# Kernel tuning notes

Hardware: AMD Instinct MI355X
Metric: run time of the kernel (lower is better)

## Reference

```python
import jax, jax.numpy as jnp
import numpy as np

B, L, V, OOV, E, H = 16, 256, 50000, 100, 128, 128
PAD_IDX, PLACEHOLDER_IDX = 0, 1


def lstm(x, W_ih, W_hh, b):
    # x: (B, T, I) -> hidden states (B, T, H); PyTorch gate order i,f,g,o
    nh = W_hh.shape[1]
    xg = jnp.einsum('bti,gi->btg', x, W_ih) + b  # precompute input gates

    def step(carry, xt):
        h, c = carry
        g = xt + h @ W_hh.T
        i, f, gg, o = jnp.split(g, 4, axis=-1)
        c = jax.nn.sigmoid(f) * c + jax.nn.sigmoid(i) * jnp.tanh(gg)
        h = jax.nn.sigmoid(o) * jnp.tanh(c)
        return (h, c), h

    bsz = x.shape[0]
    init = (jnp.zeros((bsz, nh), x.dtype), jnp.zeros((bsz, nh), x.dtype))
    _, hs = jax.lax.scan(step, init, jnp.swapaxes(xg, 0, 1))
    return jnp.swapaxes(hs, 0, 1)


def setup_inputs() -> dict:
    key = jax.random.key(0)
    ks = jax.random.split(key, 20)
    s = 0.05
    return {
        'src_tokens': jax.random.randint(ks[0], (B, L), 2, V),
        'src_lens': jnp.full((B,), L, dtype=jnp.int64 if jax.config.jax_enable_x64 else jnp.int32),
        'prev_output_tokens': jax.random.randint(ks[1], (B, 1), 2, V),
        'prev_output_lens': jnp.ones((B,), jnp.int32),
        'src_tokens_with_oov': jax.random.randint(ks[2], (B, L), 2, V + OOV),
        'oov_counts': jax.random.randint(ks[3], (B,), 0, OOV + 1),
        'decoder_state': jax.random.normal(ks[4], (B, H), jnp.float32),
        'embedding': jax.random.normal(ks[5], (V, E), jnp.float32) * 0.02,
        'enc_W_ih': jax.random.normal(ks[6], (4 * H, E), jnp.float32) * s,
        'enc_W_hh': jax.random.normal(ks[7], (4 * H, H), jnp.float32) * s,
        'enc_b': jnp.zeros((4 * H,), jnp.float32),
        'dec_W_ih': jax.random.normal(ks[8], (4 * H, E + H), jnp.float32) * s,
        'dec_W_hh': jax.random.normal(ks[9], (4 * H, H), jnp.float32) * s,
        'dec_b': jnp.zeros((4 * H,), jnp.float32),
        'attn_W': jax.random.normal(ks[10], (H, H), jnp.float32) * s,
        'out_W': jax.random.normal(ks[11], (H, 2 * H), jnp.float32) * s,
        'out_b': jnp.zeros((H,), jnp.float32),
        'copy_W': jax.random.normal(ks[12], (H, H), jnp.float32) * s,
        'gen_W': jax.random.normal(ks[13], (V + OOV, H), jnp.float32) * 0.02,
    }


def reference(src_tokens, src_lens, prev_output_tokens, prev_output_lens,
              src_tokens_with_oov, oov_counts, decoder_state,
              embedding, enc_W_ih, enc_W_hh, enc_b,
              dec_W_ih, dec_W_hh, dec_b,
              attn_W, out_W, out_b, copy_W, gen_W):
    neg_inf = -jnp.inf
    # ---- encoder ----
    enc_out = lstm(embedding[src_tokens], enc_W_ih, enc_W_hh, enc_b)  # B,L,H
    pad_mask = src_tokens == PAD_IDX                                   # B,L

    # ---- copy-state attention (selective read) ----
    mask = (prev_output_tokens == src_tokens).astype(enc_out.dtype)[..., None]  # B,L,1
    agg_w = jnp.tanh(jnp.einsum('blh,gh->blg', mask * enc_out, copy_W))
    cw = jax.nn.softmax(jnp.einsum('blg,bg->bl', agg_w, decoder_state), axis=1)
    copy_state = jnp.einsum('bl,blh->bh', cw, enc_out)

    # ---- decoder LSTM single step ----
    src_embed = embedding[prev_output_tokens[:, 0]]                    # B,E
    dec_in = jnp.concatenate([src_embed, copy_state], -1)[:, None, :]
    rnn_out = lstm(dec_in, dec_W_ih, dec_W_hh, dec_b)[:, 0]           # B,H

    # ---- attention ----
    scores = jnp.einsum('bh,blh->bl', rnn_out @ attn_W.T, enc_out)
    scores = jnp.where(pad_mask, neg_inf, scores)
    aw = jax.nn.softmax(scores, axis=1)
    ctx = jnp.einsum('bl,blh->bh', aw, enc_out)
    attn_out = jnp.tanh(jnp.concatenate([rnn_out, ctx], -1) @ out_W.T + out_b)

    # ---- generate + copy logits ----
    gen_logits = attn_out @ gen_W.T                                    # B,V+OOV
    b_idx = jnp.broadcast_to(jnp.arange(B)[:, None], (B, L))
    # scatter-reduce: equivalent to dense src_map (B, V+OOV, L) @ enc_out
    agg = jnp.zeros((B, V + OOV, H), enc_out.dtype).at[b_idx, src_tokens_with_oov].add(enc_out)
    copy_wts = jnp.tanh(jnp.einsum('bvh,gh->bvg', agg, copy_W))
    copy_score = jnp.einsum('bvg,bg->bv', copy_wts, attn_out)
    pos = jnp.arange(V + OOV)[None]
    copy_score = jnp.where(pos >= V + oov_counts[:, None], neg_inf, copy_score)

    total = gen_logits + copy_score
    total = jnp.where(pos == PLACEHOLDER_IDX, neg_inf, total)
    total_prob = jax.nn.softmax(total, axis=1)
    return total_prob, enc_out, attn_out
```

## Files before the change

### kernel.cpp

```cpp
#include <hip/hip_runtime.h>
#include <math.h>

#define B_   16
#define L_   256
#define V_   50000
#define NV_  50100
#define E_   128
#define H_   128
#define G4_  512
#define CHUNK_ 1566

typedef float f32x4 __attribute__((ext_vector_type(4)));
typedef float f32x2 __attribute__((ext_vector_type(2)));

__device__ __forceinline__ float sigm(float x){ return 1.0f/(1.0f+__expf(-x)); }
__device__ __forceinline__ float tanh_fast(float x){
  x = fminf(15.0f, fmaxf(-15.0f, x));
  float t = __expf(2.0f*x);
  return (t-1.0f)/(t+1.0f);
}

__global__ __launch_bounds__(512) void enc_xg_kernel(
    const int* __restrict__ tok, const float* __restrict__ emb,
    const float* __restrict__ Wih, const float* __restrict__ bias,
    float* __restrict__ xg)
{
  __shared__ __align__(16) float sx[16*128];
  int r0 = blockIdx.x*16;
  int t = threadIdx.x;
  for (int i=t; i<16*128; i+=512){
    int r=i>>7, e=i&127;
    sx[i] = emb[(size_t)tok[r0+r]*E_ + e];
  }
  __syncthreads();
  int g = t;
  float acc[16];
  #pragma unroll
  for (int r=0;r<16;r++) acc[r]=0.f;
  const f32x4* wr = (const f32x4*)(Wih + (size_t)g*E_);
  #pragma unroll 2
  for (int i=0;i<32;i++){
    f32x4 w = wr[i];
    #pragma unroll
    for (int r=0;r<16;r++){
      f32x4 x = ((const f32x4*)(sx + r*128))[i];
      acc[r] += w.x*x.x + w.y*x.y + w.z*x.z + w.w*x.w;
    }
  }
  float bg = bias[g];
  #pragma unroll
  for (int r=0;r<16;r++) xg[(size_t)(r0+r)*G4_ + g] = acc[r] + bg;
}

__global__ __launch_bounds__(512, 2) void enc_lstm_kernel(
    const float* __restrict__ xg, const float* __restrict__ Whh,
    float* __restrict__ enc_out)
{
  int b = blockIdx.x;
  int g = threadIdx.x;
  f32x2 w2[64];
  {
    const f32x4* wr4 = (const f32x4*)(Whh + (size_t)g*H_);
    #pragma unroll
    for (int k=0;k<32;k++){
      f32x4 wv = wr4[k];
      w2[2*k]   = wv.xy;
      w2[2*k+1] = wv.zw;
    }
  }
  #pragma unroll
  for (int k=0;k<64;k++) asm volatile("" : "+v"(w2[k]));

  __shared__ __align__(16) float sh_h[128];
  __shared__ float sh_g[512];
  if (g<128) sh_h[g]=0.f;
  float c = 0.f;
  const float* xgb = xg + (size_t)b*L_*G4_;
  float* eob = enc_out + (size_t)b*L_*H_;
  __syncthreads();

  const f32x4* sh4 = (const f32x4*)sh_h;
  bool is_gg = (g>=256 && g<384);
  float xcur = xgb[g];
  for (int t=0;t<L_;t++){
    float xnext = (t<L_-1) ? xgb[(t+1)*G4_ + g] : 0.f;
    f32x2 a0 = {xcur, 0.f}, a1 = {0.f,0.f}, a2 = {0.f,0.f}, a3 = {0.f,0.f};
    #pragma unroll
    for (int k=0;k<32;k+=4){
      f32x4 h0=sh4[k], h1=sh4[k+1], h2v=sh4[k+2], h3=sh4[k+3];
      a0 += w2[2*k+0]*h0.xy;  a1 += w2[2*k+1]*h0.zw;
      a2 += w2[2*k+2]*h1.xy;  a3 += w2[2*k+3]*h1.zw;
      a0 += w2[2*k+4]*h2v.xy; a1 += w2[2*k+5]*h2v.zw;
      a2 += w2[2*k+6]*h3.xy;  a3 += w2[2*k+7]*h3.zw;
    }
    f32x2 as = (a0+a1)+(a2+a3);
    float acc = as.x + as.y;
    float act = is_gg ? tanh_fast(acc) : sigm(acc);
    sh_g[g] = act;
    __syncthreads();
    if (g < 128){
      c = sh_g[128+g]*c + sh_g[g]*sh_g[256+g];
      float h = sh_g[384+g]*tanh_fast(c);
      sh_h[g] = h;
      eob[t*H_ + g] = h;
    }
    __syncthreads();
    xcur = xnext;
  }
}

__global__ __launch_bounds__(512) void fuse_mid_kernel(
    const int* __restrict__ src, const int* __restrict__ prev,
    const float* __restrict__ enc_out, const float* __restrict__ cW,
    const float* __restrict__ dstate, const float* __restrict__ emb,
    const float* __restrict__ dWih, const float* __restrict__ db,
    const float* __restrict__ aW, const float* __restrict__ oW,
    const float* __restrict__ ob, float* __restrict__ attn_out)
{
  int b=blockIdx.x, t=threadIdx.x;
  __shared__ float s_scopy[256];
  __shared__ int   mlist[256];
  __shared__ int   mcnt;
  __shared__ __align__(16) float se[128];
  __shared__ float sw[256];
  __shared__ float spart[512];
  __shared__ float sred[4];
  __shared__ __align__(16) float sin_[256];
  __shared__ float sg[512];
  __shared__ __align__(16) float sr[128];
  __shared__ __align__(16) float sq[128];
  __shared__ float sc[256];
  __shared__ __align__(16) float sctx[128];

  if (t==0) mcnt=0;
  __syncthreads();
  if (t<256){
    s_scopy[t]=0.f;
    if (src[b*L_+t]==prev[b]){ int i=atomicAdd(&mcnt,1); mlist[i]=t; }
  }
  __syncthreads();
  for (int mi=0; mi<mcnt; mi++){
    int l = mlist[mi];
    if (t<128) se[t] = enc_out[((size_t)b*L_+l)*H_ + t];
    __syncthreads();
    if (t<128){
      const f32x4* wr = (const f32x4*)(cW + (size_t)t*H_);
      const f32x4* e4 = (const f32x4*)se;
      float acc=0.f;
      #pragma unroll
      for (int i=0;i<32;i++){
        f32x4 wv=wr[i], e=e4[i];
        acc += wv.x*e.x + wv.y*e.y + wv.z*e.z + wv.w*e.w;
      }
      float v = tanhf(acc)*dstate[b*H_+t];
      #pragma unroll
      for (int o=32;o;o>>=1) v += __shfl_down(v,o);
      if ((t&63)==0) sred[t>>6]=v;
    }
    __syncthreads();
    if (t==0) s_scopy[l]=sred[0]+sred[1];
    __syncthreads();
  }

  float v = (t<256) ? s_scopy[t] : -INFINITY;
  {
    float m=v;
    #pragma unroll
    for (int o=32;o;o>>=1) m=fmaxf(m,__shfl_down(m,o));
    if (t<256 && (t&63)==0) sred[t>>6]=m;
  }
  __syncthreads();
  float m4 = fmaxf(fmaxf(sred[0],sred[1]),fmaxf(sred[2],sred[3]));
  __syncthreads();
  float e = (t<256) ? __expf(v-m4) : 0.f;
  {
    float z=e;
    #pragma unroll
    for (int o=32;o;o>>=1) z += __shfl_down(z,o);
    if (t<256 && (t&63)==0) sred[t>>6]=z;
  }
  __syncthreads();
  {
    float z4 = sred[0]+sred[1]+sred[2]+sred[3];
    if (t<256) sw[t] = e/z4;
  }
  __syncthreads();

  {
    int ch=t>>7, h=t&127;
    float acc=0.f;
    const float* eb = enc_out + (size_t)b*L_*H_;
    for (int l=ch*64; l<ch*64+64; l++) acc += sw[l]*eb[(size_t)l*H_+h];
    spart[t]=acc;
  }
  __syncthreads();
  if (t<128){
    float cst = spart[t]+spart[128+t]+spart[256+t]+spart[384+t];
    sin_[128+t]=cst;
    sin_[t]=emb[(size_t)prev[b]*E_+t];
  }
  __syncthreads();

  {
    const f32x4* wr=(const f32x4*)(dWih + (size_t)t*256);
    const f32x4* x4=(const f32x4*)sin_;
    f32x2 d0={db[t],0.f}, d1={0.f,0.f}, d2={0.f,0.f}, d3={0.f,0.f};
    #pragma unroll
    for (int k=0;k<64;k+=4){
      f32x4 xa=x4[k], xb=x4[k+1], xc=x4[k+2], xd=x4[k+3];
      f32x4 wa=wr[k], wb=wr[k+1], wc=wr[k+2], wd=wr[k+3];
      d0 += wa.xy*xa.xy; d1 += wa.zw*xa.zw;
      d2 += wb.xy*xb.xy; d3 += wb.zw*xb.zw;
      d0 += wc.xy*xc.xy; d1 += wc.zw*xc.zw;
      d2 += wd.xy*xd.xy; d3 += wd.zw*xd.zw;
    }
    f32x2 dsm=(d0+d1)+(d2+d3);
    sg[t]=dsm.x+dsm.y;
  }
  __syncthreads();
  if (t<128){
    float iv=sg[t], gv=sg[256+t], ov=sg[384+t];
    float cc = sigm(iv)*tanhf(gv);
    sr[t] = sigm(ov)*tanhf(cc);
  }
  __syncthreads();

  if (t<128){
    const f32x4* wr=(const f32x4*)(aW + (size_t)t*H_);
    const f32x4* x4=(const f32x4*)sr;
    float acc=0.f;
    #pragma unroll
    for (int i=0;i<32;i++){
      f32x4 wv=wr[i], x=x4[i];
      acc += wv.x*x.x + wv.y*x.y + wv.z*x.z + wv.w*x.w;
    }
    sq[t]=acc;
  }
  __syncthreads();

  if (t<256){
    const f32x4* e4=(const f32x4*)(enc_out + ((size_t)b*L_+t)*H_);
    const f32x4* q4=(const f32x4*)sq;
    float acc=0.f;
    #pragma unroll
    for (int i=0;i<32;i++){
      f32x4 ev=e4[i], q=q4[i];
      acc += ev.x*q.x + ev.y*q.y + ev.z*q.z + ev.w*q.w;
    }
    if (src[b*L_+t]==0) acc=-INFINITY;
    sc[t]=acc;
  }
  __syncthreads();

  v = (t<256) ? sc[t] : -INFINITY;
  {
    float m=v;
    #pragma unroll
    for (int o=32;o;o>>=1) m=fmaxf(m,__shfl_down(m,o));
    if (t<256 && (t&63)==0) sred[t>>6]=m;
  }
  __syncthreads();
  m4 = fmaxf(fmaxf(sred[0],sred[1]),fmaxf(sred[2],sred[3]));
  __syncthreads();
  e = (t<256) ? __expf(v-m4) : 0.f;
  {
    float z=e;
    #pragma unroll
    for (int o=32;o;o>>=1) z += __shfl_down(z,o);
    if (t<256 && (t&63)==0) sred[t>>6]=z;
  }
  __syncthreads();
  {
    float z4 = sred[0]+sred[1]+sred[2]+sred[3];
    if (t<256) sc[t] = e/z4;
  }
  __syncthreads();

  {
    int ch=t>>7, h=t&127;
    float acc=0.f;
    const float* eb = enc_out + (size_t)b*L_*H_;
    for (int l=ch*64; l<ch*64+64; l++) acc += sc[l]*eb[(size_t)l*H_+h];
    spart[t]=acc;
  }
  __syncthreads();
  if (t<128) sctx[t] = spart[t]+spart[128+t]+spart[256+t]+spart[384+t];
  __syncthreads();

  if (t<128){
    const f32x4* wr=(const f32x4*)(oW + (size_t)t*256);
    const f32x4* r4=(const f32x4*)sr;
    const f32x4* c4=(const f32x4*)sctx;
    float acc=ob[t];
    #pragma unroll
    for (int i=0;i<32;i++){
      f32x4 wv=wr[i], x=r4[i];
      acc += wv.x*x.x + wv.y*x.y + wv.z*x.z + wv.w*x.w;
    }
    #pragma unroll
    for (int i=0;i<32;i++){
      f32x4 wv=wr[32+i], x=c4[i];
      acc += wv.x*x.x + wv.y*x.y + wv.z*x.z + wv.w*x.w;
    }
    attn_out[b*H_+t]=tanhf(acc);
  }
}

__global__ __launch_bounds__(256) void copy_agg_kernel(
    const int* __restrict__ stw, const float* __restrict__ enc_out,
    float* __restrict__ agg, int* __restrict__ replist, int* __restrict__ repcnt)
{
  int b=blockIdx.x, l=threadIdx.x;
  __shared__ int stok[256];
  __shared__ int scnt;
  stok[l] = stw[b*L_+l];
  if (l==0) scnt=0;
  __syncthreads();
  int tok = stok[l];
  int first=0;
  while (stok[first]!=tok) first++;
  if (first==l){
    int myidx = atomicAdd(&scnt,1);
    f32x4 acc[32];
    #pragma unroll
    for (int i=0;i<32;i++) acc[i]=(f32x4){0.f,0.f,0.f,0.f};
    for (int l2=l; l2<L_; l2++){
      if (stok[l2]==tok){
        const f32x4* e=(const f32x4*)(enc_out + ((size_t)b*L_+l2)*H_);
        #pragma unroll
        for (int i=0;i<32;i++) acc[i]+=e[i];
      }
    }
    f32x4* dst=(f32x4*)(agg + ((size_t)b*L_+l)*H_);
    #pragma unroll
    for (int i=0;i<32;i++) dst[i]=acc[i];
    replist[b*L_+myidx]=l;
  }
  __syncthreads();
  if (l==0) repcnt[b]=scnt;
}

__global__ __launch_bounds__(256) void gen_logits_kernel(
    const float* __restrict__ attn_out, const float* __restrict__ gW,
    const int* __restrict__ oovc, float* __restrict__ total)
{
  __shared__ float sa[B_*H_];
  __shared__ float sw[64*129];
  int t=threadIdx.x;
  int v0=blockIdx.x*64;
  for (int i=t;i<B_*H_;i+=256) sa[i]=attn_out[i];
  for (int i=t;i<64*32;i+=256){
    int r=i>>5, cc=i&31;
    if (v0+r<NV_){
      float4 wv = ((const float4*)(gW + (size_t)(v0+r)*H_))[cc];
      float* dst = sw + r*129 + cc*4;
      dst[0]=wv.x; dst[1]=wv.y; dst[2]=wv.z; dst[3]=wv.w;
    }
  }
  __syncthreads();
  int vl=t&63, bq=t>>6;
  int v=v0+vl;
  if (v>=NV_) return;
  float acc[4]={0.f,0.f,0.f,0.f};
  const float* wrow = sw + vl*129;
  #pragma unroll 8
  for (int h4=0; h4<32; h4++){
    float w0=wrow[h4*4+0], w1=wrow[h4*4+1], w2=wrow[h4*4+2], w3=wrow[h4*4+3];
    #pragma unroll
    for (int k=0;k<4;k++){
      float4 a = ((const float4*)(sa + (bq*4+k)*H_))[h4];
      acc[k] += w0*a.x + w1*a.y + w2*a.z + w3*a.w;
    }
  }
  #pragma unroll
  for (int k=0;k<4;k++){
    int b=bq*4+k;
    float o = (v==1 || v >= V_ + oovc[b]) ? -INFINITY : acc[k];
    total[(size_t)b*NV_ + v] = o;
  }
}

__global__ __launch_bounds__(128) void copy_score2_kernel(
    const int* __restrict__ stw, const float* __restrict__ agg,
    const float* __restrict__ cW, const float* __restrict__ attn_out,
    const int* __restrict__ replist, const int* __restrict__ repcnt,
    float* __restrict__ total)
{
  int b=blockIdx.x;
  int cnt=repcnt[b];
  int g=threadIdx.x;
  __shared__ __align__(16) float srow[128];
  __shared__ float sred[2];
  float aog = attn_out[b*H_+g];
  f32x4 w[32];
  const f32x4* wrow=(const f32x4*)(cW + (size_t)g*H_);
  #pragma unroll
  for (int i=0;i<32;i++) w[i]=wrow[i];
  for (int ri=blockIdx.y; ri<cnt; ri+=gridDim.y){
    int l = replist[b*L_+ri];
    srow[g] = agg[((size_t)b*L_+l)*H_+g];
    __syncthreads();
    float acc=0.f;
    #pragma unroll
    for (int i=0;i<32;i++){
      f32x4 e=((const f32x4*)srow)[i]; f32x4 wv=w[i];
      acc += wv.x*e.x + wv.y*e.y + wv.z*e.z + wv.w*e.w;
    }
    float v = tanhf(acc)*aog;
    #pragma unroll
    for (int o=32;o;o>>=1) v += __shfl_down(v,o);
    if ((g&63)==0) sred[g>>6]=v;
    __syncthreads();
    if (g==0){
      int vtok = stw[b*L_+l];
      total[(size_t)b*NV_ + vtok] += sred[0]+sred[1];
    }
    __syncthreads();
  }
}

__global__ __launch_bounds__(1024) void vocab_reduce_kernel(
    const float* __restrict__ total, float* __restrict__ MZ)
{
  int b=blockIdx.x, t=threadIdx.x;
  const float* row = total + (size_t)b*NV_;
  __shared__ float sred[16];
  float m=-INFINITY;
  for (int i=t;i<NV_;i+=1024) m=fmaxf(m,row[i]);
  #pragma unroll
  for (int o=32;o;o>>=1) m=fmaxf(m,__shfl_down(m,o));
  if ((t&63)==0) sred[t>>6]=m;
  __syncthreads();
  if (t<64){
    float mm = (t<16) ? sred[t] : -INFINITY;
    #pragma unroll
    for (int o=8;o;o>>=1) mm=fmaxf(mm,__shfl_down(mm,o));
    if (t==0) sred[0]=mm;
  }
  __syncthreads();
  m = sred[0];
  float s=0.f;
  for (int i=t;i<NV_;i+=1024) s += __expf(row[i]-m);
  #pragma unroll
  for (int o=32;o;o>>=1) s += __shfl_down(s,o);
  __syncthreads();
  if ((t&63)==0) sred[t>>6]=s;
  __syncthreads();
  if (t<64){
    float ss = (t<16) ? sred[t] : 0.f;
    #pragma unroll
    for (int o=8;o;o>>=1) ss += __shfl_down(ss,o);
    if (t==0){ MZ[b]=m; MZ[16+b]=ss; }
  }
}

__global__ __launch_bounds__(256) void vocab_norm_kernel(
    float* __restrict__ total, const float* __restrict__ MZ)
{
  int b=blockIdx.x, j=blockIdx.y, t=threadIdx.x;
  int lo=j*CHUNK_, hi=min(lo+CHUNK_, NV_);
  float m=MZ[b], rz=1.0f/MZ[16+b];
  float* row = total + (size_t)b*NV_;
  for (int i=lo+t;i<hi;i+=256) row[i] = __expf(row[i]-m)*rz;
}

extern "C" void kernel_launch(void* const* d_in, const int* in_sizes, int n_in,
                              void* d_out, int out_size, void* d_ws, size_t ws_size,
                              hipStream_t stream)
{
  const int*   src_tokens = (const int*)d_in[0];
  const int*   prev_tok   = (const int*)d_in[2];
  const int*   stw        = (const int*)d_in[4];
  const int*   oovc       = (const int*)d_in[5];
  const float* dstate     = (const float*)d_in[6];
  const float* emb        = (const float*)d_in[7];
  const float* enc_Wih    = (const float*)d_in[8];
  const float* enc_Whh    = (const float*)d_in[9];
  const float* enc_b      = (const float*)d_in[10];
  const float* dec_Wih    = (const float*)d_in[11];
  const float* dec_b      = (const float*)d_in[13];
  const float* attn_W     = (const float*)d_in[14];
  const float* out_W      = (const float*)d_in[15];
  const float* out_b      = (const float*)d_in[16];
  const float* copy_W     = (const float*)d_in[17];
  const float* gen_W      = (const float*)d_in[18];

  float* out      = (float*)d_out;
  float* total    = out;
  float* enc_out  = out + (size_t)B_*NV_;
  float* attn_out = enc_out + (size_t)B_*L_*H_;

  float* ws     = (float*)d_ws;
  float* xg     = ws;
  float* agg    = xg + (size_t)B_*L_*G4_;
  float* MZ     = agg + (size_t)B_*L_*H_;
  int*   replist= (int*)(MZ + 32);
  int*   repcnt = replist + B_*L_;

  enc_xg_kernel<<<B_*L_/16, 512, 0, stream>>>(src_tokens, emb, enc_Wih, enc_b, xg);
  enc_lstm_kernel<<<B_, 512, 0, stream>>>(xg, enc_Whh, enc_out);
  fuse_mid_kernel<<<B_, 512, 0, stream>>>(src_tokens, prev_tok, enc_out, copy_W, dstate,
                                          emb, dec_Wih, dec_b, attn_W, out_W, out_b, attn_out);
  copy_agg_kernel<<<B_, 256, 0, stream>>>(stw, enc_out, agg, replist, repcnt);
  gen_logits_kernel<<<(NV_+63)/64, 256, 0, stream>>>(attn_out, gen_W, oovc, total);
  copy_score2_kernel<<<dim3(B_,32), 128, 0, stream>>>(stw, agg, copy_W, attn_out, replist, repcnt, total);
  vocab_reduce_kernel<<<B_, 1024, 0, stream>>>(total, MZ);
  vocab_norm_kernel<<<dim3(B_,32), 256, 0, stream>>>(total, MZ);
}
```

Baseline: 350.1 us.

## Halve LSTM block threads, merge copy-agg into mid kernel, split vocab softmax reduction

The encoder LSTM now runs 256 threads per block, with each thread computing two gate rows held in registers. The xg loads are prefetched two steps ahead. The copy aggregation kernel is folded into the mid kernel as 16 extra blocks so both run concurrently in one launch. The per-row vocab max/sum reduction is split across 8 chunks per row, combined with an online-softmax merge inside the normalize kernel. The goal is to cut serial launches and raise parallelism on the reduction, at the cost of higher register pressure in the recurrent loop.

```diff
diff --git a/kernel.cpp b/kernel.cpp
--- a/kernel.cpp
+++ b/kernel.cpp
@@ -8,7 +8,8 @@
 #define E_   128
 #define H_   128
 #define G4_  512
-#define CHUNK_ 1566
+#define CHUNK_  1566
+#define CHUNKP_ 6263
 
 typedef float f32x4 __attribute__((ext_vector_type(4)));
 typedef float f32x2 __attribute__((ext_vector_type(2)));
@@ -52,72 +53,125 @@
   for (int r=0;r<16;r++) xg[(size_t)(r0+r)*G4_ + g] = acc[r] + bg;
 }
 
-__global__ __launch_bounds__(512, 2) void enc_lstm_kernel(
+__global__ __launch_bounds__(256, 1) void enc_lstm_kernel(
     const float* __restrict__ xg, const float* __restrict__ Whh,
     float* __restrict__ enc_out)
 {
   int b = blockIdx.x;
-  int g = threadIdx.x;
-  f32x2 w2[64];
-  {
-    const f32x4* wr4 = (const f32x4*)(Whh + (size_t)g*H_);
-    #pragma unroll
-    for (int k=0;k<32;k++){
-      f32x4 wv = wr4[k];
-      w2[2*k]   = wv.xy;
-      w2[2*k+1] = wv.zw;
-    }
-  }
-  #pragma unroll
-  for (int k=0;k<64;k++) asm volatile("" : "+v"(w2[k]));
+  int t = threadIdx.x;
+  int g0 = t;
+  int g1 = t + 256;
+
+  f32x2 wa[64], wb[64];
+  {
+    const f32x4* wr0 = (const f32x4*)(Whh + (size_t)g0*H_);
+    const f32x4* wr1 = (const f32x4*)(Whh + (size_t)g1*H_);
+    #pragma unroll
+    for (int k=0;k<32;k++){ f32x4 v=wr0[k]; wa[2*k]=v.xy; wa[2*k+1]=v.zw; }
+    #pragma unroll
+    for (int k=0;k<32;k++){ f32x4 v=wr1[k]; wb[2*k]=v.xy; wb[2*k+1]=v.zw; }
+  }
+  #pragma unroll
+  for (int k=0;k<64;k++){ asm volatile("" : "+v"(wa[k])); asm volatile("" : "+v"(wb[k])); }
 
   __shared__ __align__(16) float sh_h[128];
   __shared__ float sh_g[512];
-  if (g<128) sh_h[g]=0.f;
+  if (t<128) sh_h[t]=0.f;
   float c = 0.f;
   const float* xgb = xg + (size_t)b*L_*G4_;
   float* eob = enc_out + (size_t)b*L_*H_;
   __syncthreads();
 
   const f32x4* sh4 = (const f32x4*)sh_h;
-  bool is_gg = (g>=256 && g<384);
-  float xcur = xgb[g];
-  for (int t=0;t<L_;t++){
-    float xnext = (t<L_-1) ? xgb[(t+1)*G4_ + g] : 0.f;
-    f32x2 a0 = {xcur, 0.f}, a1 = {0.f,0.f}, a2 = {0.f,0.f}, a3 = {0.f,0.f};
+  bool g1_tanh = (t < 128);
+
+  float xc0 = xgb[g0],        xc1 = xgb[g1];
+  float xn0 = xgb[G4_ + g0],  xn1 = xgb[G4_ + g1];
+
+  for (int s=0;s<L_;s++){
+    float xm0=0.f, xm1=0.f;
+    if (s+2 < L_){ xm0 = xgb[(size_t)(s+2)*G4_ + g0]; xm1 = xgb[(size_t)(s+2)*G4_ + g1]; }
+
+    f32x2 a0={xc0,0.f}, a1={0.f,0.f}, a2={0.f,0.f}, a3={0.f,0.f};
+    f32x2 b0={xc1,0.f}, b1={0.f,0.f}, b2={0.f,0.f}, b3={0.f,0.f};
     #pragma unroll
     for (int k=0;k<32;k+=4){
       f32x4 h0=sh4[k], h1=sh4[k+1], h2v=sh4[k+2], h3=sh4[k+3];
-      a0 += w2[2*k+0]*h0.xy;  a1 += w2[2*k+1]*h0.zw;
-      a2 += w2[2*k+2]*h1.xy;  a3 += w2[2*k+3]*h1.zw;
-      a0 += w2[2*k+4]*h2v.xy; a1 += w2[2*k+5]*h2v.zw;
-      a2 += w2[2*k+6]*h3.xy;  a3 += w2[2*k+7]*h3.zw;
-    }
-    f32x2 as = (a0+a1)+(a2+a3);
-    float acc = as.x + as.y;
-    float act = is_gg ? tanh_fast(acc) : sigm(acc);
-    sh_g[g] = act;
-    __syncthreads();
-    if (g < 128){
-      c = sh_g[128+g]*c + sh_g[g]*sh_g[256+g];
-      float h = sh_g[384+g]*tanh_fast(c);
-      sh_h[g] = h;
-      eob[t*H_ + g] = h;
-    }
-    __syncthreads();
-    xcur = xnext;
-  }
-}
-
-__global__ __launch_bounds__(512) void fuse_mid_kernel(
+      a0 += wa[2*k+0]*h0.xy;  a1 += wa[2*k+1]*h0.zw;
+      b0 += wb[2*k+0]*h0.xy;  b1 += wb[2*k+1]*h0.zw;
+      a2 += wa[2*k+2]*h1.xy;  a3 += wa[2*k+3]*h1.zw;
+      b2 += wb[2*k+2]*h1.xy;  b3 += wb[2*k+3]*h1.zw;
+      a0 += wa[2*k+4]*h2v.xy; a1 += wa[2*k+5]*h2v.zw;
+      b0 += wb[2*k+4]*h2v.xy; b1 += wb[2*k+5]*h2v.zw;
+      a2 += wa[2*k+6]*h3.xy;  a3 += wa[2*k+7]*h3.zw;
+      b2 += wb[2*k+6]*h3.xy;  b3 += wb[2*k+7]*h3.zw;
+    }
+    f32x2 as=(a0+a1)+(a2+a3);
+    f32x2 bs=(b0+b1)+(b2+b3);
+    float acc0 = as.x+as.y;
+    float acc1 = bs.x+bs.y;
+    sh_g[g0] = sigm(acc0);
+    sh_g[g1] = g1_tanh ? tanh_fast(acc1) : sigm(acc1);
+    __syncthreads();
+    if (t < 128){
+      c = sh_g[128+t]*c + sh_g[t]*sh_g[256+t];
+      float h = sh_g[384+t]*tanh_fast(c);
+      sh_h[t] = h;
+      eob[(size_t)s*H_ + t] = h;
+    }
+    __syncthreads();
+    xc0=xn0; xc1=xn1; xn0=xm0; xn1=xm1;
+    #pragma unroll
+    for (int k=0;k<64;k++){ asm volatile("" : "+v"(wa[k])); asm volatile("" : "+v"(wb[k])); }
+  }
+}
+
+__global__ __launch_bounds__(512) void midagg_kernel(
     const int* __restrict__ src, const int* __restrict__ prev,
     const float* __restrict__ enc_out, const float* __restrict__ cW,
     const float* __restrict__ dstate, const float* __restrict__ emb,
     const float* __restrict__ dWih, const float* __restrict__ db,
     const float* __restrict__ aW, const float* __restrict__ oW,
-    const float* __restrict__ ob, float* __restrict__ attn_out)
-{
-  int b=blockIdx.x, t=threadIdx.x;
+    const float* __restrict__ ob, float* __restrict__ attn_out,
+    const int* __restrict__ stw, float* __restrict__ agg,
+    int* __restrict__ replist, int* __restrict__ repcnt)
+{
+  int t=threadIdx.x;
+  if (blockIdx.x >= 16){
+    int b = blockIdx.x - 16;
+    __shared__ int stok[256];
+    __shared__ int scnt;
+    if (t<256) stok[t] = stw[b*L_+t];
+    if (t==0) scnt=0;
+    __syncthreads();
+    if (t<256){
+      int tok = stok[t];
+      int first=0;
+      while (stok[first]!=tok) first++;
+      if (first==t){
+        int myidx = atomicAdd(&scnt,1);
+        f32x4 acc[32];
+        #pragma unroll
+        for (int i=0;i<32;i++) acc[i]=(f32x4){0.f,0.f,0.f,0.f};
+        for (int l2=t; l2<L_; l2++){
+          if (stok[l2]==tok){
+            const f32x4* e=(const f32x4*)(enc_out + ((size_t)b*L_+l2)*H_);
+            #pragma unroll
+            for (int i=0;i<32;i++) acc[i]+=e[i];
+          }
+        }
+        f32x4* dst=(f32x4*)(agg + ((size_t)b*L_+t)*H_);
+        #pragma unroll
+        for (int i=0;i<32;i++) dst[i]=acc[i];
+        replist[b*L_+myidx]=t;
+      }
+    }
+    __syncthreads();
+    if (t==0) repcnt[b]=scnt;
+    return;
+  }
+
+  int b=blockIdx.x;
   __shared__ float s_scopy[256];
   __shared__ int   mlist[256];
   __shared__ int   mcnt;
@@ -208,11 +262,11 @@
     #pragma unroll
     for (int k=0;k<64;k+=4){
       f32x4 xa=x4[k], xb=x4[k+1], xc=x4[k+2], xd=x4[k+3];
-      f32x4 wa=wr[k], wb=wr[k+1], wc=wr[k+2], wd=wr[k+3];
-      d0 += wa.xy*xa.xy; d1 += wa.zw*xa.zw;
-      d2 += wb.xy*xb.xy; d3 += wb.zw*xb.zw;
-      d0 += wc.xy*xc.xy; d1 += wc.zw*xc.zw;
-      d2 += wd.xy*xd.xy; d3 += wd.zw*xd.zw;
+      f32x4 wva=wr[k], wvb=wr[k+1], wvc=wr[k+2], wvd=wr[k+3];
+      d0 += wva.xy*xa.xy; d1 += wva.zw*xa.zw;
+      d2 += wvb.xy*xb.xy; d3 += wvb.zw*xb.zw;
+      d0 += wvc.xy*xc.xy; d1 += wvc.zw*xc.zw;
+      d2 += wvd.xy*xd.xy; d3 += wvd.zw*xd.zw;
     }
     f32x2 dsm=(d0+d1)+(d2+d3);
     sg[t]=dsm.x+dsm.y;
@@ -304,40 +358,6 @@
     }
     attn_out[b*H_+t]=tanhf(acc);
   }
-}
-
-__global__ __launch_bounds__(256) void copy_agg_kernel(
-    const int* __restrict__ stw, const float* __restrict__ enc_out,
-    float* __restrict__ agg, int* __restrict__ replist, int* __restrict__ repcnt)
-{
-  int b=blockIdx.x, l=threadIdx.x;
-  __shared__ int stok[256];
-  __shared__ int scnt;
-  stok[l] = stw[b*L_+l];
-  if (l==0) scnt=0;
-  __syncthreads();
-  int tok = stok[l];
-  int first=0;
-  while (stok[first]!=tok) first++;
-  if (first==l){
-    int myidx = atomicAdd(&scnt,1);
-    f32x4 acc[32];
-    #pragma unroll
-    for (int i=0;i<32;i++) acc[i]=(f32x4){0.f,0.f,0.f,0.f};
-    for (int l2=l; l2<L_; l2++){
-      if (stok[l2]==tok){
-        const f32x4* e=(const f32x4*)(enc_out + ((size_t)b*L_+l2)*H_);
-        #pragma unroll
-        for (int i=0;i<32;i++) acc[i]+=e[i];
-      }
-    }
-    f32x4* dst=(f32x4*)(agg + ((size_t)b*L_+l)*H_);
-    #pragma unroll
-    for (int i=0;i<32;i++) dst[i]=acc[i];
-    replist[b*L_+myidx]=l;
-  }
-  __syncthreads();
-  if (l==0) repcnt[b]=scnt;
 }
 
 __global__ __launch_bounds__(256) void gen_logits_kernel(
@@ -419,49 +439,50 @@
   }
 }
 
-__global__ __launch_bounds__(1024) void vocab_reduce_kernel(
-    const float* __restrict__ total, float* __restrict__ MZ)
-{
-  int b=blockIdx.x, t=threadIdx.x;
+__global__ __launch_bounds__(256) void vocab_pass1_kernel(
+    const float* __restrict__ total, float* __restrict__ pmax, float* __restrict__ psum)
+{
+  int b=blockIdx.x, j=blockIdx.y, t=threadIdx.x;
+  int lo=j*CHUNKP_, hi=min(lo+CHUNKP_, NV_);
   const float* row = total + (size_t)b*NV_;
-  __shared__ float sred[16];
+  __shared__ float sred[4];
   float m=-INFINITY;
-  for (int i=t;i<NV_;i+=1024) m=fmaxf(m,row[i]);
+  for (int i=lo+t;i<hi;i+=256) m=fmaxf(m,row[i]);
   #pragma unroll
   for (int o=32;o;o>>=1) m=fmaxf(m,__shfl_down(m,o));
   if ((t&63)==0) sred[t>>6]=m;
   __syncthreads();
-  if (t<64){
-    float mm = (t<16) ? sred[t] : -INFINITY;
-    #pragma unroll
-    for (int o=8;o;o>>=1) mm=fmaxf(mm,__shfl_down(mm,o));
-    if (t==0) sred[0]=mm;
-  }
-  __syncthreads();
-  m = sred[0];
+  m = fmaxf(fmaxf(sred[0],sred[1]),fmaxf(sred[2],sred[3]));
+  __syncthreads();
   float s=0.f;
-  for (int i=t;i<NV_;i+=1024) s += __expf(row[i]-m);
+  if (m > -INFINITY){
+    for (int i=lo+t;i<hi;i+=256) s += __expf(row[i]-m);
+  }
   #pragma unroll
   for (int o=32;o;o>>=1) s += __shfl_down(s,o);
-  __syncthreads();
   if ((t&63)==0) sred[t>>6]=s;
   __syncthreads();
-  if (t<64){
-    float ss = (t<16) ? sred[t] : 0.f;
-    #pragma unroll
-    for (int o=8;o;o>>=1) ss += __shfl_down(ss,o);
-    if (t==0){ MZ[b]=m; MZ[16+b]=ss; }
-  }
+  if (t==0){ pmax[b*8+j]=m; psum[b*8+j]=sred[0]+sred[1]+sred[2]+sred[3]; }
 }
 
 __global__ __launch_bounds__(256) void vocab_norm_kernel(
-    float* __restrict__ total, const float* __restrict__ MZ)
+    float* __restrict__ total, const float* __restrict__ pmax,
+    const float* __restrict__ psum)
 {
   int b=blockIdx.x, j=blockIdx.y, t=threadIdx.x;
+  float M=-INFINITY;
+  #pragma unroll
+  for (int k=0;k<8;k++) M=fmaxf(M,pmax[b*8+k]);
+  float Z=0.f;
+  #pragma unroll
+  for (int k=0;k<8;k++){
+    float pj=pmax[b*8+k];
+    Z += (pj > -INFINITY) ? psum[b*8+k]*__expf(pj-M) : 0.f;
+  }
+  float rz=1.0f/Z;
   int lo=j*CHUNK_, hi=min(lo+CHUNK_, NV_);
-  float m=MZ[b], rz=1.0f/MZ[16+b];
   float* row = total + (size_t)b*NV_;
-  for (int i=lo+t;i<hi;i+=256) row[i] = __expf(row[i]-m)*rz;
+  for (int i=lo+t;i<hi;i+=256) row[i] = __expf(row[i]-M)*rz;
 }
 
 extern "C" void kernel_launch(void* const* d_in, const int* in_sizes, int n_in,
@@ -493,17 +514,18 @@
   float* ws     = (float*)d_ws;
   float* xg     = ws;
   float* agg    = xg + (size_t)B_*L_*G4_;
-  float* MZ     = agg + (size_t)B_*L_*H_;
-  int*   replist= (int*)(MZ + 32);
+  float* pmax   = agg + (size_t)B_*L_*H_;
+  float* psum   = pmax + 128;
+  int*   replist= (int*)(psum + 128);
   int*   repcnt = replist + B_*L_;
 
   enc_xg_kernel<<<B_*L_/16, 512, 0, stream>>>(src_tokens, emb, enc_Wih, enc_b, xg);
-  enc_lstm_kernel<<<B_, 512, 0, stream>>>(xg, enc_Whh, enc_out);
-  fuse_mid_kernel<<<B_, 512, 0, stream>>>(src_tokens, prev_tok, enc_out, copy_W, dstate,
-                                          emb, dec_Wih, dec_b, attn_W, out_W, out_b, attn_out);
-  copy_agg_kernel<<<B_, 256, 0, stream>>>(stw, enc_out, agg, replist, repcnt);
+  enc_lstm_kernel<<<B_, 256, 0, stream>>>(xg, enc_Whh, enc_out);
+  midagg_kernel<<<32, 512, 0, stream>>>(src_tokens, prev_tok, enc_out, copy_W, dstate,
+                                        emb, dec_Wih, dec_b, attn_W, out_W, out_b, attn_out,
+                                        stw, agg, replist, repcnt);
   gen_logits_kernel<<<(NV_+63)/64, 256, 0, stream>>>(attn_out, gen_W, oovc, total);
   copy_score2_kernel<<<dim3(B_,32), 128, 0, stream>>>(stw, agg, copy_W, attn_out, replist, repcnt, total);
-  vocab_reduce_kernel<<<B_, 1024, 0, stream>>>(total, MZ);
-  vocab_norm_kernel<<<dim3(B_,32), 256, 0, stream>>>(total, MZ);
-}
+  vocab_pass1_kernel<<<dim3(B_,8), 256, 0, stream>>>(total, pmax, psum);
+  vocab_norm_kernel<<<dim3(B_,32), 256, 0, stream>>>(total, pmax, psum);
+}
```

After: 533.3 us. 52.3% more time.
